# Optimization experiments

Hardware: AMD Instinct MI355X
Metric: run time of the kernel (lower is better)

Reference implementation:

```python
import jax, jax.numpy as jnp
import numpy as np

N, D = 100000, 32      # rows / columns of dist & angle
H, W = 100000, 32      # rows / columns of index matrices
NUM_CLASSES = 22       # size of the eye() one-hot table


def setup_inputs() -> dict:
    key = jax.random.key(0)
    k1, k2, k3, k4, k5 = jax.random.split(key, 5)
    dist = jax.random.uniform(k1, (N, D), dtype=jnp.float32)
    angle = jax.random.uniform(k2, (N, D), dtype=jnp.float32)
    idx_t = jax.random.randint(k3, (H, W), 0, NUM_CLASSES, dtype=jnp.int32)
    index_t = jax.random.randint(k4, (H, W), 0, D + 1, dtype=jnp.int32)
    index_h = jax.random.randint(k5, (H,), 0, N, dtype=jnp.int32)
    return {"dist": dist, "angle": angle, "idx_t": idx_t,
            "index_t": index_t, "index_h": index_h}


def reference(dist, angle, idx_t, index_t, index_h):
    n = dist.shape[0]
    # append a zero column so index D acts as a padding sentinel
    zcol = jnp.zeros((n, 1), dtype=dist.dtype)
    dist_new = jnp.concatenate([dist, zcol], axis=1)    # [N, D+1]
    angle_new = jnp.concatenate([angle, zcol], axis=1)  # [N, D+1]

    h, w = idx_t.shape
    # torch builds ab = index_h @ ones(1, w); equivalent to a broadcast
    ab = jnp.broadcast_to(index_h[:, None], (h, w))     # [h, w]

    dist_t = dist_new[ab, index_t]    # [h, w] gather
    angle_t = angle_new[ab, index_t]  # [h, w] gather

    # eye(22)[idx_t] one-hot lookup, flattened per row -> [h, 22*w]
    x1 = jax.nn.one_hot(idx_t, NUM_CLASSES, dtype=dist.dtype).reshape(h, -1)

    # global min-max normalize of the gathered distances
    dmin = dist_t.min()
    dmax = dist_t.max()
    dist_n = (dist_t - dmin) / (dmax - dmin)

    # [h, 22*w + w + w]
    return jnp.concatenate([x1, dist_n, angle_t], axis=1)
```

## Files before the change

kernel.cpp:

```cpp
#include <hip/hip_runtime.h>

#define DCOLS 32
#define WCOLS 32
#define NUM_CLASSES 22
#define ONEHOT_COLS (NUM_CLASSES * WCOLS)
#define OUT_COLS (ONEHOT_COLS + WCOLS + WCOLS)
#define ROWS_PER_BLOCK 8

typedef float vfloat4 __attribute__((ext_vector_type(4)));


__global__ __launch_bounds__(256) void minmax_kernel(
    const float* __restrict__ dist,
    const int*   __restrict__ index_t,
    const int*   __restrict__ index_h,
    unsigned*    __restrict__ ws,
    int total4)
{
    float vmin = __int_as_float(0x7f800000);
    float vmax = 0.0f;
    const int stride = gridDim.x * blockDim.x;
    for (int i4 = blockIdx.x * blockDim.x + threadIdx.x; i4 < total4; i4 += stride) {
        const int4 it = reinterpret_cast<const int4*>(index_t)[i4];
        const int  h  = i4 >> 3;
        const int  row = index_h[h] * DCOLS;
        float v0 = 0.0f, v1 = 0.0f, v2 = 0.0f, v3 = 0.0f;
        if (it.x < DCOLS) v0 = dist[row + it.x];
        if (it.y < DCOLS) v1 = dist[row + it.y];
        if (it.z < DCOLS) v2 = dist[row + it.z];
        if (it.w < DCOLS) v3 = dist[row + it.w];
        vmin = fminf(fminf(fminf(vmin, v0), fminf(v1, v2)), v3);
        vmax = fmaxf(fmaxf(fmaxf(vmax, v0), fmaxf(v1, v2)), v3);
    }
    #pragma unroll
    for (int off = 32; off > 0; off >>= 1) {
        vmin = fminf(vmin, __shfl_down(vmin, off, 64));
        vmax = fmaxf(vmax, __shfl_down(vmax, off, 64));
    }
    __shared__ float smin[4], smax[4];
    const int lane = threadIdx.x & 63;
    const int wave = threadIdx.x >> 6;
    if (lane == 0) { smin[wave] = vmin; smax[wave] = vmax; }
    __syncthreads();
    if (threadIdx.x == 0) {
        float m = smin[0], M = smax[0];
        #pragma unroll
        for (int k = 1; k < 4; ++k) { m = fminf(m, smin[k]); M = fmaxf(M, smax[k]); }
        atomicMin(ws,             __float_as_uint(-m));
        atomicMax((int*)(ws + 1), __float_as_int(M));
    }
}

__global__ __launch_bounds__(256) void fill_kernel(
    const float* __restrict__ dist,
    const float* __restrict__ angle,
    const int*   __restrict__ idx_t,
    const int*   __restrict__ index_t,
    const int*   __restrict__ index_h,
    const unsigned* __restrict__ ws,
    float*       __restrict__ out,
    int H)
{
    const int h0  = blockIdx.x * ROWS_PER_BLOCK;
    const int tid = threadIdx.x;

    __shared__ int   s_idx[ROWS_PER_BLOCK][WCOLS];
    __shared__ float s_dist[ROWS_PER_BLOCK][WCOLS];
    __shared__ float s_angle[ROWS_PER_BLOCK][WCOLS];

    {
        const float dmin = -__uint_as_float(ws[0]);
        const float dmax =  __uint_as_float(ws[1]);
        const float inv  = 1.0f / (dmax - dmin);
        const int r = tid >> 5;
        const int c = tid & 31;
        const int h = h0 + r;
        if (h < H) {
            const int it = index_t[h * WCOLS + c];
            s_idx[r][c] = idx_t[h * WCOLS + c];
            float dv = 0.0f, av = 0.0f;
            if (it < DCOLS) {
                const int base = index_h[h] * DCOLS;
                dv = dist[base + it];
                av = angle[base + it];
            }
            s_dist[r][c]  = (dv - dmin) * inv;
            s_angle[r][c] = av;
        }
    }
    __syncthreads();

    const bool full = (h0 + ROWS_PER_BLOCK) <= H;
    #pragma unroll
    for (int m = 0; m < 6; ++m) {
        const int t    = m * 256 + tid;
        const int row  = t / 192;
        const int col4 = t - row * 192;
        const int j0   = col4 * 4;
        vfloat4 v4;
        #pragma unroll
        for (int k = 0; k < 4; ++k) {
            const int j = j0 + k;
            float v;
            if (j < ONEHOT_COLS) {
                const int w = j / NUM_CLASSES;
                const int c = j - w * NUM_CLASSES;
                v = (s_idx[row][w] == c) ? 1.0f : 0.0f;
            } else if (j < ONEHOT_COLS + WCOLS) {
                v = s_dist[row][j - ONEHOT_COLS];
            } else {
                v = s_angle[row][j - (ONEHOT_COLS + WCOLS)];
            }
            v4[k] = v;
        }
        if (full) {
            vfloat4* o = reinterpret_cast<vfloat4*>(out + (size_t)h0 * OUT_COLS);
            __builtin_nontemporal_store(v4, o + t);
        } else if (h0 + row < H) {
            vfloat4* o = reinterpret_cast<vfloat4*>(out + (size_t)(h0 + row) * OUT_COLS);
            __builtin_nontemporal_store(v4, o + col4);
        }
    }
}

extern "C" void kernel_launch(void* const* d_in, const int* in_sizes, int n_in,
                              void* d_out, int out_size, void* d_ws, size_t ws_size,
                              hipStream_t stream) {
    const float* dist    = (const float*)d_in[0];
    const float* angle   = (const float*)d_in[1];
    const int*   idx_t   = (const int*)d_in[2];
    const int*   index_t = (const int*)d_in[3];
    const int*   index_h = (const int*)d_in[4];
    float*       out     = (float*)d_out;
    unsigned*    ws      = (unsigned*)d_ws;

    const int H      = in_sizes[4];
    const int total4 = (H * WCOLS) / 4;

    (void)hipMemsetAsync(ws, 0xFF, 8, stream);

    hipLaunchKernelGGL(minmax_kernel, dim3(1024), dim3(256), 0, stream,
                       dist, index_t, index_h, ws, total4);

    const int fill_blocks = (H + ROWS_PER_BLOCK - 1) / ROWS_PER_BLOCK;
    hipLaunchKernelGGL(fill_kernel, dim3(fill_blocks), dim3(256), 0, stream,
                       dist, angle, idx_t, index_t, index_h, ws, out, H);
}
```

Measured before the change: 373.5 us.

## Fuse min-max and fill into one cooperative kernel with grid sync

Replaces the separate min-max reduction kernel and fill kernel with a single cooperative kernel. It writes the one-hot and angle columns while gathering the distances, keeps each thread's raw distances in registers, and after a grid-wide sync writes only the normalized distance column. This removes the second pass over index_t and dist and one launch. In exchange it relies on a grid sync across 1024 blocks, a fixed MAXCHUNKS limit that assumes H fits within 13 chunks per block, and scattered scalar stores for the distance column.

```diff
diff --git a/kernel.cpp b/kernel.cpp
--- a/kernel.cpp
+++ b/kernel.cpp
@@ -1,124 +1,136 @@
 #include <hip/hip_runtime.h>
+#include <hip/hip_cooperative_groups.h>
+
+namespace cg = cooperative_groups;
 
 #define DCOLS 32
 #define WCOLS 32
 #define NUM_CLASSES 22
 #define ONEHOT_COLS (NUM_CLASSES * WCOLS)
 #define OUT_COLS (ONEHOT_COLS + WCOLS + WCOLS)
-#define ROWS_PER_BLOCK 8
+#define ROWS_PER_CHUNK 8
+#define NBLOCKS 1024
+#define MAXCHUNKS 13
 
 typedef float vfloat4 __attribute__((ext_vector_type(4)));
 
-
-__global__ __launch_bounds__(256) void minmax_kernel(
+__global__ __launch_bounds__(256, 4) void fused_kernel(
     const float* __restrict__ dist,
+    const float* __restrict__ angle,
+    const int*   __restrict__ idx_t,
     const int*   __restrict__ index_t,
     const int*   __restrict__ index_h,
     unsigned*    __restrict__ ws,
-    int total4)
+    float*       __restrict__ out,
+    int H)
 {
+    const int tid = threadIdx.x;
+    const int r   = tid >> 5;
+    const int c   = tid & 31;
+    const int nchunks = (H + ROWS_PER_CHUNK - 1) / ROWS_PER_CHUNK;
+
+    __shared__ int   s_idx[ROWS_PER_CHUNK][WCOLS];
+    __shared__ float s_angle[ROWS_PER_CHUNK][WCOLS];
+    __shared__ float smin[4], smax[4];
+    __shared__ unsigned s_mm[2];
+
+    float dstash[MAXCHUNKS];
     float vmin = __int_as_float(0x7f800000);
     float vmax = 0.0f;
-    const int stride = gridDim.x * blockDim.x;
-    for (int i4 = blockIdx.x * blockDim.x + threadIdx.x; i4 < total4; i4 += stride) {
-        const int4 it = reinterpret_cast<const int4*>(index_t)[i4];
-        const int  h  = i4 >> 3;
-        const int  row = index_h[h] * DCOLS;
-        float v0 = 0.0f, v1 = 0.0f, v2 = 0.0f, v3 = 0.0f;
-        if (it.x < DCOLS) v0 = dist[row + it.x];
-        if (it.y < DCOLS) v1 = dist[row + it.y];
-        if (it.z < DCOLS) v2 = dist[row + it.z];
-        if (it.w < DCOLS) v3 = dist[row + it.w];
-        vmin = fminf(fminf(fminf(vmin, v0), fminf(v1, v2)), v3);
-        vmax = fmaxf(fmaxf(fmaxf(vmax, v0), fmaxf(v1, v2)), v3);
+
+    #pragma unroll
+    for (int ci = 0; ci < MAXCHUNKS; ++ci) {
+        const int chunk = blockIdx.x + ci * gridDim.x;
+        if (chunk >= nchunks) break;
+        const int h0 = chunk * ROWS_PER_CHUNK;
+        const int h  = h0 + r;
+
+        float dv = 0.0f, av = 0.0f;
+        int   ii = 0;
+        if (h < H) {
+            ii = idx_t[h * WCOLS + c];
+            const int it = index_t[h * WCOLS + c];
+            if (it < DCOLS) {
+                const int base = index_h[h] * DCOLS;
+                dv = dist[base + it];
+                av = angle[base + it];
+            }
+            vmin = fminf(vmin, dv);
+            vmax = fmaxf(vmax, dv);
+        }
+        s_idx[r][c]   = ii;
+        s_angle[r][c] = av;
+        dstash[ci]    = dv;
+        __syncthreads();
+
+        const bool full = (h0 + ROWS_PER_CHUNK) <= H;
+        #pragma unroll
+        for (int m = 0; m < 6; ++m) {
+            const int t    = m * 256 + tid;
+            const int row  = t / 192;
+            const int col4 = t - row * 192;
+            if (col4 >= 176 && col4 < 184) continue;
+            const int j0 = col4 * 4;
+            vfloat4 v4;
+            #pragma unroll
+            for (int k = 0; k < 4; ++k) {
+                const int j = j0 + k;
+                float v;
+                if (j < ONEHOT_COLS) {
+                    const int w  = j / NUM_CLASSES;
+                    const int cc = j - w * NUM_CLASSES;
+                    v = (s_idx[row][w] == cc) ? 1.0f : 0.0f;
+                } else {
+                    v = s_angle[row][j - (ONEHOT_COLS + WCOLS)];
+                }
+                v4[k] = v;
+            }
+            if (full || (h0 + row) < H) {
+                vfloat4* o = reinterpret_cast<vfloat4*>(
+                    out + (size_t)(h0 + row) * OUT_COLS);
+                __builtin_nontemporal_store(v4, o + col4);
+            }
+        }
+        __syncthreads();
     }
+
     #pragma unroll
     for (int off = 32; off > 0; off >>= 1) {
         vmin = fminf(vmin, __shfl_down(vmin, off, 64));
         vmax = fmaxf(vmax, __shfl_down(vmax, off, 64));
     }
-    __shared__ float smin[4], smax[4];
-    const int lane = threadIdx.x & 63;
-    const int wave = threadIdx.x >> 6;
+    const int lane = tid & 63;
+    const int wave = tid >> 6;
     if (lane == 0) { smin[wave] = vmin; smax[wave] = vmax; }
     __syncthreads();
-    if (threadIdx.x == 0) {
+    if (tid == 0) {
         float m = smin[0], M = smax[0];
         #pragma unroll
         for (int k = 1; k < 4; ++k) { m = fminf(m, smin[k]); M = fmaxf(M, smax[k]); }
         atomicMin(ws,             __float_as_uint(-m));
         atomicMax((int*)(ws + 1), __float_as_int(M));
     }
-}
 
-__global__ __launch_bounds__(256) void fill_kernel(
-    const float* __restrict__ dist,
-    const float* __restrict__ angle,
-    const int*   __restrict__ idx_t,
-    const int*   __restrict__ index_t,
-    const int*   __restrict__ index_h,
-    const unsigned* __restrict__ ws,
-    float*       __restrict__ out,
-    int H)
-{
-    const int h0  = blockIdx.x * ROWS_PER_BLOCK;
-    const int tid = threadIdx.x;
+    cg::this_grid().sync();
 
-    __shared__ int   s_idx[ROWS_PER_BLOCK][WCOLS];
-    __shared__ float s_dist[ROWS_PER_BLOCK][WCOLS];
-    __shared__ float s_angle[ROWS_PER_BLOCK][WCOLS];
-
-    {
-        const float dmin = -__uint_as_float(ws[0]);
-        const float dmax =  __uint_as_float(ws[1]);
-        const float inv  = 1.0f / (dmax - dmin);
-        const int r = tid >> 5;
-        const int c = tid & 31;
-        const int h = h0 + r;
-        if (h < H) {
-            const int it = index_t[h * WCOLS + c];
-            s_idx[r][c] = idx_t[h * WCOLS + c];
-            float dv = 0.0f, av = 0.0f;
-            if (it < DCOLS) {
-                const int base = index_h[h] * DCOLS;
-                dv = dist[base + it];
-                av = angle[base + it];
-            }
-            s_dist[r][c]  = (dv - dmin) * inv;
-            s_angle[r][c] = av;
-        }
+    if (tid == 0) {
+        s_mm[0] = atomicOr(ws, 0u);
+        s_mm[1] = atomicOr(ws + 1, 0u);
     }
     __syncthreads();
+    const float dmin = -__uint_as_float(s_mm[0]);
+    const float dmax =  __uint_as_float(s_mm[1]);
+    const float inv  = 1.0f / (dmax - dmin);
 
-    const bool full = (h0 + ROWS_PER_BLOCK) <= H;
     #pragma unroll
-    for (int m = 0; m < 6; ++m) {
-        const int t    = m * 256 + tid;
-        const int row  = t / 192;
-        const int col4 = t - row * 192;
-        const int j0   = col4 * 4;
-        vfloat4 v4;
-        #pragma unroll
-        for (int k = 0; k < 4; ++k) {
-            const int j = j0 + k;
-            float v;
-            if (j < ONEHOT_COLS) {
-                const int w = j / NUM_CLASSES;
-                const int c = j - w * NUM_CLASSES;
-                v = (s_idx[row][w] == c) ? 1.0f : 0.0f;
-            } else if (j < ONEHOT_COLS + WCOLS) {
-                v = s_dist[row][j - ONEHOT_COLS];
-            } else {
-                v = s_angle[row][j - (ONEHOT_COLS + WCOLS)];
-            }
-            v4[k] = v;
-        }
-        if (full) {
-            vfloat4* o = reinterpret_cast<vfloat4*>(out + (size_t)h0 * OUT_COLS);
-            __builtin_nontemporal_store(v4, o + t);
-        } else if (h0 + row < H) {
-            vfloat4* o = reinterpret_cast<vfloat4*>(out + (size_t)(h0 + row) * OUT_COLS);
-            __builtin_nontemporal_store(v4, o + col4);
+    for (int ci = 0; ci < MAXCHUNKS; ++ci) {
+        const int chunk = blockIdx.x + ci * gridDim.x;
+        if (chunk >= nchunks) break;
+        const int h = chunk * ROWS_PER_CHUNK + r;
+        if (h < H) {
+            __builtin_nontemporal_store(
+                (dstash[ci] - dmin) * inv,
+                out + (size_t)h * OUT_COLS + ONEHOT_COLS + c);
         }
     }
 }
@@ -133,16 +145,13 @@
     const int*   index_h = (const int*)d_in[4];
     float*       out     = (float*)d_out;
     unsigned*    ws      = (unsigned*)d_ws;
-
-    const int H      = in_sizes[4];
-    const int total4 = (H * WCOLS) / 4;
+    int          H       = in_sizes[4];
 
     (void)hipMemsetAsync(ws, 0xFF, 8, stream);
 
-    hipLaunchKernelGGL(minmax_kernel, dim3(1024), dim3(256), 0, stream,
-                       dist, index_t, index_h, ws, total4);
-
-    const int fill_blocks = (H + ROWS_PER_BLOCK - 1) / ROWS_PER_BLOCK;
-    hipLaunchKernelGGL(fill_kernel, dim3(fill_blocks), dim3(256), 0, stream,
-                       dist, angle, idx_t, index_t, index_h, ws, out, H);
+    void* args[] = {(void*)&dist, (void*)&angle, (void*)&idx_t, (void*)&index_t,
+                    (void*)&index_h, (void*)&ws, (void*)&out, (void*)&H};
+    (void)hipLaunchCooperativeKernel((const void*)fused_kernel,
+                                     dim3(NBLOCKS), dim3(256),
+                                     args, 0, stream);
 }
```

Result: slower. 511.1 us (+36.8%).

## Fuse min-max reduction into fill pass and patch normalized distances afterward

Applied to the files above, without the earlier changes.

Removes the separate min-max pre-pass by computing the block min/max inside the main fill kernel. That kernel writes the one-hot and angle columns directly and stashes the raw gathered distances in the workspace. A small second kernel then normalizes the stashed distances and writes them into the distance columns. This saves a second gather over index_t/index_h/dist, but adds an extra write and read of the stash plus a strided partial write into the output.

```diff
diff --git a/kernel.cpp b/kernel.cpp
--- a/kernel.cpp
+++ b/kernel.cpp
@@ -10,54 +10,14 @@
 typedef float vfloat4 __attribute__((ext_vector_type(4)));
 
 
-__global__ __launch_bounds__(256) void minmax_kernel(
-    const float* __restrict__ dist,
-    const int*   __restrict__ index_t,
-    const int*   __restrict__ index_h,
-    unsigned*    __restrict__ ws,
-    int total4)
-{
-    float vmin = __int_as_float(0x7f800000);
-    float vmax = 0.0f;
-    const int stride = gridDim.x * blockDim.x;
-    for (int i4 = blockIdx.x * blockDim.x + threadIdx.x; i4 < total4; i4 += stride) {
-        const int4 it = reinterpret_cast<const int4*>(index_t)[i4];
-        const int  h  = i4 >> 3;
-        const int  row = index_h[h] * DCOLS;
-        float v0 = 0.0f, v1 = 0.0f, v2 = 0.0f, v3 = 0.0f;
-        if (it.x < DCOLS) v0 = dist[row + it.x];
-        if (it.y < DCOLS) v1 = dist[row + it.y];
-        if (it.z < DCOLS) v2 = dist[row + it.z];
-        if (it.w < DCOLS) v3 = dist[row + it.w];
-        vmin = fminf(fminf(fminf(vmin, v0), fminf(v1, v2)), v3);
-        vmax = fmaxf(fmaxf(fmaxf(vmax, v0), fmaxf(v1, v2)), v3);
-    }
-    #pragma unroll
-    for (int off = 32; off > 0; off >>= 1) {
-        vmin = fminf(vmin, __shfl_down(vmin, off, 64));
-        vmax = fmaxf(vmax, __shfl_down(vmax, off, 64));
-    }
-    __shared__ float smin[4], smax[4];
-    const int lane = threadIdx.x & 63;
-    const int wave = threadIdx.x >> 6;
-    if (lane == 0) { smin[wave] = vmin; smax[wave] = vmax; }
-    __syncthreads();
-    if (threadIdx.x == 0) {
-        float m = smin[0], M = smax[0];
-        #pragma unroll
-        for (int k = 1; k < 4; ++k) { m = fminf(m, smin[k]); M = fmaxf(M, smax[k]); }
-        atomicMin(ws,             __float_as_uint(-m));
-        atomicMax((int*)(ws + 1), __float_as_int(M));
-    }
-}
-
-__global__ __launch_bounds__(256) void fill_kernel(
+__global__ __launch_bounds__(256) void fill_a_kernel(
     const float* __restrict__ dist,
     const float* __restrict__ angle,
     const int*   __restrict__ idx_t,
     const int*   __restrict__ index_t,
     const int*   __restrict__ index_h,
-    const unsigned* __restrict__ ws,
+    unsigned*    __restrict__ ws,
+    float*       __restrict__ stash,
     float*       __restrict__ out,
     int H)
 {
@@ -65,28 +25,31 @@
     const int tid = threadIdx.x;
 
     __shared__ int   s_idx[ROWS_PER_BLOCK][WCOLS];
-    __shared__ float s_dist[ROWS_PER_BLOCK][WCOLS];
     __shared__ float s_angle[ROWS_PER_BLOCK][WCOLS];
+    __shared__ float smin[4], smax[4];
 
+    float vmin = __int_as_float(0x7f800000);
+    float vmax = 0.0f;
     {
-        const float dmin = -__uint_as_float(ws[0]);
-        const float dmax =  __uint_as_float(ws[1]);
-        const float inv  = 1.0f / (dmax - dmin);
         const int r = tid >> 5;
         const int c = tid & 31;
         const int h = h0 + r;
+        float dv = 0.0f, av = 0.0f;
+        int   ii = 0;
         if (h < H) {
+            ii = idx_t[h * WCOLS + c];
             const int it = index_t[h * WCOLS + c];
-            s_idx[r][c] = idx_t[h * WCOLS + c];
-            float dv = 0.0f, av = 0.0f;
             if (it < DCOLS) {
                 const int base = index_h[h] * DCOLS;
                 dv = dist[base + it];
                 av = angle[base + it];
             }
-            s_dist[r][c]  = (dv - dmin) * inv;
-            s_angle[r][c] = av;
+            vmin = fminf(vmin, dv);
+            vmax = fmaxf(vmax, dv);
+            stash[h * WCOLS + c] = dv;
         }
+        s_idx[r][c]   = ii;
+        s_angle[r][c] = av;
     }
     __syncthreads();
 
@@ -96,31 +59,65 @@
         const int t    = m * 256 + tid;
         const int row  = t / 192;
         const int col4 = t - row * 192;
-        const int j0   = col4 * 4;
+        if (col4 >= 176 && col4 < 184) continue;
+        const int j0 = col4 * 4;
         vfloat4 v4;
         #pragma unroll
         for (int k = 0; k < 4; ++k) {
             const int j = j0 + k;
             float v;
             if (j < ONEHOT_COLS) {
-                const int w = j / NUM_CLASSES;
-                const int c = j - w * NUM_CLASSES;
-                v = (s_idx[row][w] == c) ? 1.0f : 0.0f;
-            } else if (j < ONEHOT_COLS + WCOLS) {
-                v = s_dist[row][j - ONEHOT_COLS];
+                const int w  = j / NUM_CLASSES;
+                const int cc = j - w * NUM_CLASSES;
+                v = (s_idx[row][w] == cc) ? 1.0f : 0.0f;
             } else {
                 v = s_angle[row][j - (ONEHOT_COLS + WCOLS)];
             }
             v4[k] = v;
         }
-        if (full) {
-            vfloat4* o = reinterpret_cast<vfloat4*>(out + (size_t)h0 * OUT_COLS);
-            __builtin_nontemporal_store(v4, o + t);
-        } else if (h0 + row < H) {
-            vfloat4* o = reinterpret_cast<vfloat4*>(out + (size_t)(h0 + row) * OUT_COLS);
+        if (full || (h0 + row) < H) {
+            vfloat4* o = reinterpret_cast<vfloat4*>(
+                out + (size_t)(h0 + row) * OUT_COLS);
             __builtin_nontemporal_store(v4, o + col4);
         }
     }
+
+    #pragma unroll
+    for (int off = 32; off > 0; off >>= 1) {
+        vmin = fminf(vmin, __shfl_down(vmin, off, 64));
+        vmax = fmaxf(vmax, __shfl_down(vmax, off, 64));
+    }
+    const int lane = tid & 63;
+    const int wave = tid >> 6;
+    if (lane == 0) { smin[wave] = vmin; smax[wave] = vmax; }
+    __syncthreads();
+    if (tid == 0) {
+        float m = smin[0], M = smax[0];
+        #pragma unroll
+        for (int k = 1; k < 4; ++k) { m = fminf(m, smin[k]); M = fmaxf(M, smax[k]); }
+        atomicMin(ws,             __float_as_uint(-m));
+        atomicMax((int*)(ws + 1), __float_as_int(M));
+    }
+}
+
+__global__ __launch_bounds__(256) void fill_b_kernel(
+    const float*    __restrict__ stash,
+    const unsigned* __restrict__ ws,
+    float*          __restrict__ out,
+    int total4)
+{
+    const int i = blockIdx.x * blockDim.x + threadIdx.x;
+    if (i >= total4) return;
+    const float dmin = -__uint_as_float(ws[0]);
+    const float dmax =  __uint_as_float(ws[1]);
+    const float inv  = 1.0f / (dmax - dmin);
+
+    vfloat4 v = reinterpret_cast<const vfloat4*>(stash)[i];
+    v = (v - dmin) * inv;
+    const int row  = i >> 3;
+    const int col4 = i & 7;
+    vfloat4* o = reinterpret_cast<vfloat4*>(out + (size_t)row * OUT_COLS);
+    __builtin_nontemporal_store(v, o + 176 + col4);
 }
 
 extern "C" void kernel_launch(void* const* d_in, const int* in_sizes, int n_in,
@@ -133,16 +130,17 @@
     const int*   index_h = (const int*)d_in[4];
     float*       out     = (float*)d_out;
     unsigned*    ws      = (unsigned*)d_ws;
-
-    const int H      = in_sizes[4];
-    const int total4 = (H * WCOLS) / 4;
+    float*       stash   = (float*)((char*)d_ws + 256);
+    const int    H       = in_sizes[4];
 
     (void)hipMemsetAsync(ws, 0xFF, 8, stream);
 
-    hipLaunchKernelGGL(minmax_kernel, dim3(1024), dim3(256), 0, stream,
-                       dist, index_t, index_h, ws, total4);
+    const int blocks_a = (H + ROWS_PER_BLOCK - 1) / ROWS_PER_BLOCK;
+    hipLaunchKernelGGL(fill_a_kernel, dim3(blocks_a), dim3(256), 0, stream,
+                       dist, angle, idx_t, index_t, index_h, ws, stash, out, H);
 
-    const int fill_blocks = (H + ROWS_PER_BLOCK - 1) / ROWS_PER_BLOCK;
-    hipLaunchKernelGGL(fill_kernel, dim3(fill_blocks), dim3(256), 0, stream,
-                       dist, angle, idx_t, index_t, index_h, ws, out, H);
+    const int total4   = (H * WCOLS) / 4;
+    const int blocks_b = (total4 + 255) / 256;
+    hipLaunchKernelGGL(fill_b_kernel, dim3(blocks_b), dim3(256), 0, stream,
+                       stash, ws, out, total4);
 }
```

Result: slower. 572.6 us (+53.3%).

## Split fill kernel into independent one-hot and gather-normalize kernels

Applied to the files above, without the earlier changes.

The fused fill kernel is split in two. One kernel writes only the one-hot region of each output row, and a separate kernel writes the normalized dist and angle columns with scalar stores. The intent is to let the one-hot writes avoid loading dist, angle and index data. However, the one-hot kernel is still launched after minmax on the same stream, so it cannot overlap with it, and it also writes zeros into the last 64 columns that the gather kernel then overwrites. This adds redundant writes, an extra launch and re-reads of index_t.

```diff
diff --git a/kernel.cpp b/kernel.cpp
--- a/kernel.cpp
+++ b/kernel.cpp
@@ -5,10 +5,58 @@
 #define NUM_CLASSES 22
 #define ONEHOT_COLS (NUM_CLASSES * WCOLS)
 #define OUT_COLS (ONEHOT_COLS + WCOLS + WCOLS)
-#define ROWS_PER_BLOCK 8
+#define ROWS_A 8
+#define ROWS_B 4
 
 typedef float vfloat4 __attribute__((ext_vector_type(4)));
 
+
+__global__ __launch_bounds__(256) void onehot_kernel(
+    const int* __restrict__ idx_t,
+    float*     __restrict__ out,
+    int H)
+{
+    const int h0  = blockIdx.x * ROWS_A;
+    const int tid = threadIdx.x;
+
+    __shared__ int s_idx[ROWS_A][WCOLS];
+    {
+        const int r = tid >> 5;
+        const int c = tid & 31;
+        const int h = h0 + r;
+        s_idx[r][c] = (h < H) ? idx_t[h * WCOLS + c] : 0;
+    }
+    __syncthreads();
+
+    const bool full = (h0 + ROWS_A) <= H;
+    #pragma unroll
+    for (int m = 0; m < 6; ++m) {
+        const int t    = m * 256 + tid;
+        const int row  = t / 192;
+        const int col4 = t - row * 192;
+        const int j0   = col4 * 4;
+        vfloat4 v4;
+        #pragma unroll
+        for (int k = 0; k < 4; ++k) {
+            const int j = j0 + k;
+            float v = 0.0f;
+            if (j < ONEHOT_COLS) {
+                const int w  = j / NUM_CLASSES;
+                const int cc = j - w * NUM_CLASSES;
+                v = (s_idx[row][w] == cc) ? 1.0f : 0.0f;
+            }
+            v4[k] = v;
+        }
+        if (full) {
+            vfloat4* o = reinterpret_cast<vfloat4*>(out + (size_t)h0 * OUT_COLS);
+            __builtin_nontemporal_store(v4, o + t);
+        } else if (h0 + row < H) {
+            vfloat4* o = reinterpret_cast<vfloat4*>(
+                out + (size_t)(h0 + row) * OUT_COLS);
+            __builtin_nontemporal_store(v4, o + col4);
+        }
+    }
+}
 
 __global__ __launch_bounds__(256) void minmax_kernel(
     const float* __restrict__ dist,
@@ -51,76 +99,33 @@
     }
 }
 
-__global__ __launch_bounds__(256) void fill_kernel(
+__global__ __launch_bounds__(256) void gather_kernel(
     const float* __restrict__ dist,
     const float* __restrict__ angle,
-    const int*   __restrict__ idx_t,
     const int*   __restrict__ index_t,
     const int*   __restrict__ index_h,
     const unsigned* __restrict__ ws,
     float*       __restrict__ out,
     int H)
 {
-    const int h0  = blockIdx.x * ROWS_PER_BLOCK;
     const int tid = threadIdx.x;
+    const int h   = blockIdx.x * ROWS_B + (tid >> 6);
+    const int cc  = tid & 63;
+    if (h >= H) return;
 
-    __shared__ int   s_idx[ROWS_PER_BLOCK][WCOLS];
-    __shared__ float s_dist[ROWS_PER_BLOCK][WCOLS];
-    __shared__ float s_angle[ROWS_PER_BLOCK][WCOLS];
+    const float dmin = -__uint_as_float(ws[0]);
+    const float dmax =  __uint_as_float(ws[1]);
+    const float inv  = 1.0f / (dmax - dmin);
 
-    {
-        const float dmin = -__uint_as_float(ws[0]);
-        const float dmax =  __uint_as_float(ws[1]);
-        const float inv  = 1.0f / (dmax - dmin);
-        const int r = tid >> 5;
-        const int c = tid & 31;
-        const int h = h0 + r;
-        if (h < H) {
-            const int it = index_t[h * WCOLS + c];
-            s_idx[r][c] = idx_t[h * WCOLS + c];
-            float dv = 0.0f, av = 0.0f;
-            if (it < DCOLS) {
-                const int base = index_h[h] * DCOLS;
-                dv = dist[base + it];
-                av = angle[base + it];
-            }
-            s_dist[r][c]  = (dv - dmin) * inv;
-            s_angle[r][c] = av;
-        }
+    const int it = index_t[h * WCOLS + (cc & 31)];
+    float v = 0.0f;
+    if (it < DCOLS) {
+        const int base = index_h[h] * DCOLS;
+        v = (cc < 32) ? dist[base + it] : angle[base + it];
     }
-    __syncthreads();
-
-    const bool full = (h0 + ROWS_PER_BLOCK) <= H;
-    #pragma unroll
-    for (int m = 0; m < 6; ++m) {
-        const int t    = m * 256 + tid;
-        const int row  = t / 192;
-        const int col4 = t - row * 192;
-        const int j0   = col4 * 4;
-        vfloat4 v4;
-        #pragma unroll
-        for (int k = 0; k < 4; ++k) {
-            const int j = j0 + k;
-            float v;
-            if (j < ONEHOT_COLS) {
-                const int w = j / NUM_CLASSES;
-                const int c = j - w * NUM_CLASSES;
-                v = (s_idx[row][w] == c) ? 1.0f : 0.0f;
-            } else if (j < ONEHOT_COLS + WCOLS) {
-                v = s_dist[row][j - ONEHOT_COLS];
-            } else {
-                v = s_angle[row][j - (ONEHOT_COLS + WCOLS)];
-            }
-            v4[k] = v;
-        }
-        if (full) {
-            vfloat4* o = reinterpret_cast<vfloat4*>(out + (size_t)h0 * OUT_COLS);
-            __builtin_nontemporal_store(v4, o + t);
-        } else if (h0 + row < H) {
-            vfloat4* o = reinterpret_cast<vfloat4*>(out + (size_t)(h0 + row) * OUT_COLS);
-            __builtin_nontemporal_store(v4, o + col4);
-        }
-    }
+    if (cc < 32) v = (v - dmin) * inv;
+    __builtin_nontemporal_store(
+        v, out + (size_t)h * OUT_COLS + ONEHOT_COLS + cc);
 }
 
 extern "C" void kernel_launch(void* const* d_in, const int* in_sizes, int n_in,
@@ -133,16 +138,19 @@
     const int*   index_h = (const int*)d_in[4];
     float*       out     = (float*)d_out;
     unsigned*    ws      = (unsigned*)d_ws;
-
-    const int H      = in_sizes[4];
-    const int total4 = (H * WCOLS) / 4;
+    const int    H       = in_sizes[4];
 
     (void)hipMemsetAsync(ws, 0xFF, 8, stream);
 
+    const int total4 = (H * WCOLS) / 4;
     hipLaunchKernelGGL(minmax_kernel, dim3(1024), dim3(256), 0, stream,
                        dist, index_t, index_h, ws, total4);
 
-    const int fill_blocks = (H + ROWS_PER_BLOCK - 1) / ROWS_PER_BLOCK;
-    hipLaunchKernelGGL(fill_kernel, dim3(fill_blocks), dim3(256), 0, stream,
-                       dist, angle, idx_t, index_t, index_h, ws, out, H);
+    const int blocks_a = (H + ROWS_A - 1) / ROWS_A;
+    hipLaunchKernelGGL(onehot_kernel, dim3(blocks_a), dim3(256), 0, stream,
+                       idx_t, out, H);
+
+    const int blocks_b = (H + ROWS_B - 1) / ROWS_B;
+    hipLaunchKernelGGL(gather_kernel, dim3(blocks_b), dim3(256), 0, stream,
+                       dist, angle, index_t, index_h, ws, out, H);
 }
```

New measurement: 393.9 us. 1.05x slower.
